# Kernel tuning notes

Hardware: AMD Instinct MI355X
Metric: run time of the kernel (lower is better)

The kernel has to match this reference:

```python
import jax, jax.numpy as jnp
import numpy as np

B, C, H, W = 16, 256, 32, 32
EPS = 1e-6


def setup_inputs() -> dict:
    key = jax.random.key(0)
    ks = jax.random.split(key, 6)
    s = 1.0 / np.sqrt(C)  # conv-like init scale
    return {
        "x": jax.random.normal(ks[0], (B, C, H, W), dtype=jnp.float32),
        "ln_w": jnp.ones((C,), dtype=jnp.float32),
        "ln_b": jnp.zeros((C,), dtype=jnp.float32),
        "wq": jax.random.normal(ks[1], (C, C), dtype=jnp.float32) * s,
        "bq": jnp.zeros((C,), dtype=jnp.float32),
        "wk": jax.random.normal(ks[2], (C, C), dtype=jnp.float32) * s,
        "bk": jnp.zeros((C,), dtype=jnp.float32),
        "wv": jax.random.normal(ks[3], (C, C), dtype=jnp.float32) * s,
        "bv": jnp.zeros((C,), dtype=jnp.float32),
        "wp": jax.random.normal(ks[4], (C, C), dtype=jnp.float32) * s,
        "bp": jnp.zeros((C,), dtype=jnp.float32),
    }


def reference(x, ln_w, ln_b, wq, bq, wk, bk, wv, bv, wp, bp):
    b, c, h, w = x.shape
    n = h * w
    # LayerNorm2d: normalize over channel dim (biased variance)
    mean = jnp.mean(x, axis=1, keepdims=True)
    var = jnp.var(x, axis=1, keepdims=True)
    hn = (x - mean) / jnp.sqrt(var + EPS)
    hn = hn * ln_w[None, :, None, None] + ln_b[None, :, None, None]
    hn = hn.reshape(b, c, n)  # [B, C, N]
    # 1x1 convs == channel matmuls; tokens layout [B, N, C]
    q = jnp.einsum('oc,bcn->bno', wq, hn) + bq  # [B, N, C]
    k = jnp.einsum('oc,bcn->bon', wk, hn) + bk[None, :, None]  # [B, C, N]
    v = jnp.einsum('oc,bcn->bno', wv, hn) + bv  # [B, N, C]
    scale = c ** (-0.5)
    attn = jnp.einsum('bnc,bcm->bnm', q, k) * scale  # [B, N, N]
    attn = jax.nn.softmax(attn, axis=-1)
    # dropout is identity in eval mode (deterministic reference)
    out = jnp.einsum('bnm,bmc->bnc', attn, v)  # [B, N, C]
    out = jnp.einsum('oc,bnc->bon', wp, out) + bp[None, :, None]  # [B, C, N]
    out = out.reshape(b, c, h, w)
    return x + out
```

## Files before the change

kernel.cpp:

```cpp
#include <hip/hip_runtime.h>
#include <hip/hip_bf16.h>
#include <stdint.h>
#include <math.h>

typedef __attribute__((ext_vector_type(8))) short bf8_t;
typedef __attribute__((ext_vector_type(4))) float f4_t;
typedef __attribute__((ext_vector_type(16))) float f16x_t;
typedef __attribute__((ext_vector_type(2))) unsigned u32x2;
typedef unsigned short u16;

#define GLOAD16(g, l) __builtin_amdgcn_global_load_lds(                                  \
    (const __attribute__((address_space(1))) void*)(g),                                  \
    (__attribute__((address_space(3))) void*)(l), 16, 0, 0)

#define KEEPALIVE(v) asm volatile("" : "+v"(v))

#define QSCALE 0.090168444f

__device__ __forceinline__ u16 f2bf(float f) {
    union { float f; unsigned u; } c; c.f = f;
    unsigned u = c.u;
    return (u16)((u + 0x7fffu + ((u >> 16) & 1u)) >> 16);
}

__device__ __forceinline__ unsigned cvt_pk_bf16(float lo, float hi_) {
    unsigned r;
    asm("v_cvt_pk_bf16_f32 %0, %1, %2" : "=v"(r) : "v"(lo), "v"(hi_));
    return r;
}

__device__ __forceinline__ void plswap(unsigned& a, unsigned& b) {
    u32x2 r = __builtin_amdgcn_permlane32_swap(a, b, false, false);
    a = r[0]; b = r[1];
}

__device__ __forceinline__ void pack_frags(const unsigned* pw, bf8_t& f0v, bf8_t& f1v) {
    unsigned w0 = pw[0], w1 = pw[1], w2 = pw[2], w3 = pw[3];
    unsigned u0 = pw[4], u1 = pw[5], u2 = pw[6], u3 = pw[7];
    plswap(w2, w0);
    plswap(w3, w1);
    plswap(u2, u0);
    plswap(u3, u1);
    union { unsigned w[4]; bf8_t v; } f0, f1;
    f0.w[0] = w0; f0.w[1] = w1; f0.w[2] = w2; f0.w[3] = w3;
    f1.w[0] = u0; f1.w[1] = u1; f1.w[2] = u2; f1.w[3] = u3;
    f0v = f0.v; f1v = f1.v;
}

__global__ void prep_kernel(const float* __restrict__ wq, const float* __restrict__ wk,
                            const float* __restrict__ wv, const float* __restrict__ wp,
                            const float* __restrict__ bq, const float* __restrict__ bk,
                            const float* __restrict__ bv,
                            u16* __restrict__ wcatT, u16* __restrict__ wpt,
                            float* __restrict__ biasc) {
    int idx = blockIdx.x * 256 + threadIdx.x;
    if (idx < 196608) {
        int o = idx >> 8, c = idx & 255;
        float v = (o < 256) ? wq[o * 256 + c]
                : (o < 512) ? wk[(o - 256) * 256 + c]
                            : wv[(o - 512) * 256 + c];
        wcatT[(((c >> 3) * 768) + o) * 8 + (c & 7)] = f2bf(v);
    } else if (idx < 262144) {
        int i = idx - 196608;
        int o = i >> 8, d = i & 255;
        wpt[(((d >> 3) * 256) + o) * 8 + (d & 7)] = f2bf(wp[i]);
    } else if (idx < 262912) {
        int i = idx - 262144;
        biasc[i] = (i < 256) ? bq[i] : (i < 512) ? bk[i - 256] : bv[i - 512];
    }
}

__global__ __launch_bounds__(256) void lnqkv_kernel(
    const float* __restrict__ x, const float* __restrict__ lw,
    const float* __restrict__ lb,
    const u16* __restrict__ wcatT, const float* __restrict__ biasc,
    u16* __restrict__ qbuf, u16* __restrict__ ktp, u16* __restrict__ vtp) {
    __shared__ u16 hn_lds[32 * 32 * 8];
    __shared__ float2 red[8][32];

    const int tid = threadIdx.x;
    const int bid = blockIdx.x;
    const int b = bid >> 5, n0 = (bid & 31) * 32;
    const int tok = tid & 31, cpart = tid >> 5;

    const float* xb = x + (size_t)b * 262144 + n0 + tok;
    float v[32];
    float s = 0.f, s2 = 0.f;
    #pragma unroll
    for (int i = 0; i < 32; i++) {
        v[i] = xb[(size_t)(cpart * 32 + i) * 1024];
        s += v[i]; s2 += v[i] * v[i];
    }
    red[cpart][tok] = make_float2(s, s2);
    __syncthreads();
    s = 0.f; s2 = 0.f;
    #pragma unroll
    for (int gi = 0; gi < 8; gi++) { float2 p = red[gi][tok]; s += p.x; s2 += p.y; }
    float mean = s * 0.00390625f;
    float rstd = rsqrtf(s2 * 0.00390625f - mean * mean + 1e-6f);
    #pragma unroll
    for (int j = 0; j < 4; j++) {
        bf8_t pk;
        #pragma unroll
        for (int e = 0; e < 8; e++) {
            int c = cpart * 32 + j * 8 + e;
            pk[e] = (short)f2bf((v[j * 8 + e] - mean) * rstd * lw[c] + lb[c]);
        }
        *(bf8_t*)&hn_lds[((cpart * 4 + j) * 32 + tok) * 8] = pk;
    }
    __syncthreads();

    const int lane = tid & 63, wv_ = tid >> 6;
    const int hi = lane >> 5, lq = lane & 31;
    const int n = n0 + lq;

    bf8_t hnf[16];
    #pragma unroll
    for (int tc = 0; tc < 16; tc++)
        hnf[tc] = *(const bf8_t*)&hn_lds[((tc * 2 + hi) * 32 + lq) * 8];
    #pragma unroll
    for (int tc = 0; tc < 16; tc++) KEEPALIVE(hnf[tc]);

    #pragma unroll
    for (int grp = 0; grp < 3; grp++) {
        #pragma unroll
        for (int sub = 0; sub < 2; sub++) {
            const int cb = grp * 256 + (wv_ * 2 + sub) * 32;
            bf8_t wf[16];
            #pragma unroll
            for (int tc = 0; tc < 16; tc++)
                wf[tc] = *(const bf8_t*)(wcatT + (((size_t)(tc * 2 + hi) * 768) + cb + lq) * 8);
            f16x_t acc = (f16x_t)0.0f;
            if (grp < 2) {
                #pragma unroll
                for (int tc = 0; tc < 16; tc++)
                    acc = __builtin_amdgcn_mfma_f32_32x32x16_bf16(wf[tc], hnf[tc], acc, 0, 0, 0);
                #pragma unroll
                for (int r = 0; r < 16; r++) {
                    float bv = biasc[cb + (r & 3) + 8 * (r >> 2) + 4 * hi];
                    acc[r] += bv;
                    if (grp == 0) acc[r] *= QSCALE;
                }
            } else {
                #pragma unroll
                for (int tc = 0; tc < 16; tc++)
                    acc = __builtin_amdgcn_mfma_f32_32x32x16_bf16(hnf[tc], wf[tc], acc, 0, 0, 0);
                float bv = biasc[cb + lq];
                #pragma unroll
                for (int r = 0; r < 16; r++) acc[r] += bv;
            }

            unsigned pw[8];
            #pragma unroll
            for (int j = 0; j < 8; j++) pw[j] = cvt_pk_bf16(acc[2 * j], acc[2 * j + 1]);
            bf8_t f0v, f1v;
            pack_frags(pw, f0v, f1v);

            if (grp == 0) {
                u16* qb = &qbuf[((size_t)b * 1024 + n) * 256 + cb];
                *(bf8_t*)(qb + hi * 8) = f0v;
                *(bf8_t*)(qb + 16 + hi * 8) = f1v;
            } else if (grp == 1) {
                int c0 = cb - 256 + hi * 8;
                *(bf8_t*)&ktp[(((size_t)b * 32 + (c0 >> 3)) * 1024 + n) * 8] = f0v;
                int c1 = c0 + 16;
                *(bf8_t*)&ktp[(((size_t)b * 32 + (c1 >> 3)) * 1024 + n) * 8] = f1v;
            } else {
                int d = cb - 512 + lq;
                int t0 = n0 + hi * 8;
                *(bf8_t*)&vtp[(((size_t)b * 128 + (t0 >> 3)) * 256 + d) * 8] = f0v;
                int t1 = t0 + 16;
                *(bf8_t*)&vtp[(((size_t)b * 128 + (t1 >> 3)) * 256 + d) * 8] = f1v;
            }
        }
    }
}

__global__ __launch_bounds__(512)
__attribute__((amdgpu_waves_per_eu(2, 2)))
void flash_kernel(const u16* __restrict__ qbuf,
                  const u16* __restrict__ kt,
                  const u16* __restrict__ vt3,
                  const u16* __restrict__ wpt,
                  const float* __restrict__ bp,
                  const float* __restrict__ x,
                  float* __restrict__ out) {
    __shared__ u16 K_lds[2][2][32 * 32 * 8];
    __shared__ u16 V_lds[2][2][4 * 256 * 8];
    __shared__ float lstat[2][32];

    const int flat = blockIdx.x;
    const int xcd = flat & 7, idx = flat >> 3;
    const int b = (xcd << 1) | (idx & 1);
    const int qb = idx >> 1;
    const int tid = threadIdx.x;
    const int wv = tid >> 6, lane = tid & 63;
    const int hi = lane >> 5, lq = lane & 31;
    const int qw = wv & 1, dw = (wv >> 1) & 1, g = wv >> 2;

    const int qrow = qb * 64 + qw * 32 + lq;
    const u16* qptr = qbuf + (size_t)(b * 1024 + qrow) * 256 + hi * 8;
    bf8_t qf[16];
    #pragma unroll
    for (int tc = 0; tc < 16; tc++) qf[tc] = *(const bf8_t*)(qptr + tc * 16);

    float l_r = 0.f;
    f16x_t o_acc[4];
    #pragma unroll
    for (int dt = 0; dt < 4; dt++) o_acc[dt] = (f16x_t)0.0f;

#define STAGE(T, BUF)                                                                     \
    {                                                                                     \
        _Pragma("unroll")                                                                 \
        for (int g2 = 0; g2 < 2; g2++) {                                                  \
            _Pragma("unroll")                                                             \
            for (int it = 0; it < 2; it++) {                                              \
                int cid = it * 512 + tid;                                                 \
                int chunk = cid >> 5, kvl = cid & 31;                                     \
                const u16* gk = kt + (((size_t)b * 32 + chunk) * 1024                     \
                                      + g2 * 512 + (T) * 32 + kvl) * 8;                   \
                GLOAD16(gk, &K_lds[g2][BUF][cid * 8]);                                    \
            }                                                                             \
            _Pragma("unroll")                                                             \
            for (int it = 0; it < 2; it++) {                                              \
                int cid = it * 512 + tid;                                                 \
                int kc = cid >> 8, d = cid & 255;                                         \
                const u16* gv = vt3 + (((size_t)b * 128 + g2 * 64 + (T) * 4 + kc) * 256   \
                                       + d) * 8;                                          \
                GLOAD16(gv, &V_lds[g2][BUF][cid * 8]);                                    \
            }                                                                             \
        }                                                                                 \
    }

    STAGE(0, 0);
    STAGE(1, 1);
    asm volatile("s_waitcnt vmcnt(8)" ::: "memory");
    __builtin_amdgcn_s_barrier();

    for (int t = 0; t < 16; ++t) {
        const int buf = t & 1;

        const u16* kb = &K_lds[g][buf][0];
        bf8_t kf[16];
        #pragma unroll
        for (int tc = 0; tc < 16; tc++)
            kf[tc] = *(const bf8_t*)(kb + ((tc * 2 + hi) * 32 + lq) * 8);
        #pragma unroll
        for (int tc = 0; tc < 16; tc++) KEEPALIVE(kf[tc]);

        f16x_t s0 = (f16x_t)0.0f, s1 = (f16x_t)0.0f;
        __builtin_amdgcn_s_setprio(1);
        #pragma unroll
        for (int tc = 0; tc < 8; tc++) {
            s0 = __builtin_amdgcn_mfma_f32_32x32x16_bf16(kf[2 * tc],     qf[2 * tc],     s0, 0, 0, 0);
            s1 = __builtin_amdgcn_mfma_f32_32x32x16_bf16(kf[2 * tc + 1], qf[2 * tc + 1], s1, 0, 0, 0);
        }
        __builtin_amdgcn_s_setprio(0);

        const u16* vb = &V_lds[g][buf][0];
        bf8_t vf[8];
        #pragma unroll
        for (int dt = 0; dt < 4; dt++) {
            int vrow = dw * 128 + dt * 32 + lq;
            vf[2 * dt]     = *(const bf8_t*)(vb + (hi * 256 + vrow) * 8);
            vf[2 * dt + 1] = *(const bf8_t*)(vb + ((2 + hi) * 256 + vrow) * 8);
        }
        #pragma unroll
        for (int j = 0; j < 8; j++) KEEPALIVE(vf[j]);

        f16x_t s = s0 + s1;

        float sum = 0.f;
        #pragma unroll
        for (int r = 0; r < 16; r++) { s[r] = exp2f(s[r]); sum += s[r]; }
        l_r += sum;

        unsigned pw[8];
        #pragma unroll
        for (int j = 0; j < 8; j++) pw[j] = cvt_pk_bf16(s[2 * j], s[2 * j + 1]);
        bf8_t f0v, f1v;
        pack_frags(pw, f0v, f1v);

        asm volatile("s_waitcnt lgkmcnt(0)" ::: "memory");
        __builtin_amdgcn_s_barrier();
        if (t < 14) STAGE(t + 2, buf);

        __builtin_amdgcn_s_setprio(1);
        #pragma unroll
        for (int dt = 0; dt < 4; dt++) {
            o_acc[dt] = __builtin_amdgcn_mfma_f32_32x32x16_bf16(vf[2 * dt],     f0v, o_acc[dt], 0, 0, 0);
            o_acc[dt] = __builtin_amdgcn_mfma_f32_32x32x16_bf16(vf[2 * dt + 1], f1v, o_acc[dt], 0, 0, 0);
        }
        __builtin_amdgcn_s_setprio(0);

        if (t < 15) {
            if (t < 14) { asm volatile("s_waitcnt vmcnt(8)" ::: "memory"); }
            else        { asm volatile("s_waitcnt vmcnt(0)" ::: "memory"); }
            __builtin_amdgcn_s_barrier();
        }
    }

    __syncthreads();

    float l_tot = l_r + __shfl_xor(l_r, 32);
    float* obuf = (float*)&K_lds[0][0][0];
    float* rb = obuf + (qw * 2 + dw) * 4096;
    if (g == 1) {
        #pragma unroll
        for (int dt = 0; dt < 4; dt++)
            #pragma unroll
            for (int r = 0; r < 16; r++) {
                int drow = dt * 32 + (r & 3) + 8 * (r >> 2) + 4 * hi;
                rb[drow * 32 + lq] = o_acc[dt][r];
            }
        if (dw == 0 && hi == 0) lstat[qw][lq] = l_tot;
    }
    __syncthreads();

    bf8_t wpf[16];
    #pragma unroll
    for (int tc = 0; tc < 16; tc++)
        wpf[tc] = *(const bf8_t*)(wpt + (((tc * 2 + hi) * 256) + wv * 32 + lq) * 8);

    u16* O16 = (u16*)&V_lds[0][0][0];
    if (g == 0) {
        float inv = 1.0f / (l_tot + lstat[qw][lq]);
        #pragma unroll
        for (int dt = 0; dt < 4; dt++)
            #pragma unroll
            for (int r = 0; r < 16; r++) {
                int drow = dt * 32 + (r & 3) + 8 * (r >> 2) + 4 * hi;
                int d = dw * 128 + drow;
                float val = (o_acc[dt][r] + rb[drow * 32 + lq]) * inv;
                O16[((d >> 3) * 64 + qw * 32 + lq) * 8 + (d & 7)] = f2bf(val);
            }
    }
    __syncthreads();

    f16x_t p0 = (f16x_t)0.0f, p1 = (f16x_t)0.0f;
    __builtin_amdgcn_s_setprio(1);
    #pragma unroll
    for (int tc = 0; tc < 16; tc++) {
        bf8_t of0 = *(const bf8_t*)(O16 + ((tc * 2 + hi) * 64 + lq) * 8);
        bf8_t of1 = *(const bf8_t*)(O16 + ((tc * 2 + hi) * 64 + 32 + lq) * 8);
        p0 = __builtin_amdgcn_mfma_f32_32x32x16_bf16(wpf[tc], of0, p0, 0, 0, 0);
        p1 = __builtin_amdgcn_mfma_f32_32x32x16_bf16(wpf[tc], of1, p1, 0, 0, 0);
    }
    __builtin_amdgcn_s_setprio(0);
    #pragma unroll
    for (int r = 0; r < 16; r++) {
        int crow = wv * 32 + (r & 3) + 8 * (r >> 2) + 4 * hi;
        size_t base = ((size_t)b * 256 + crow) * 1024 + qb * 64;
        float bpv = bp[crow];
        out[base + lq]      = p0[r] + bpv + x[base + lq];
        out[base + 32 + lq] = p1[r] + bpv + x[base + 32 + lq];
    }
#undef STAGE
}

extern "C" void kernel_launch(void* const* d_in, const int* in_sizes, int n_in,
                              void* d_out, int out_size, void* d_ws, size_t ws_size,
                              hipStream_t stream) {
    (void)in_sizes; (void)n_in; (void)out_size; (void)ws_size;
    const float* x   = (const float*)d_in[0];
    const float* lnw = (const float*)d_in[1];
    const float* lnb = (const float*)d_in[2];
    const float* wq  = (const float*)d_in[3];
    const float* bq  = (const float*)d_in[4];
    const float* wk  = (const float*)d_in[5];
    const float* bk  = (const float*)d_in[6];
    const float* wv  = (const float*)d_in[7];
    const float* bv  = (const float*)d_in[8];
    const float* wp  = (const float*)d_in[9];
    const float* bp  = (const float*)d_in[10];
    float* out = (float*)d_out;

    char* ws = (char*)d_ws;
    u16*   wcatT = (u16*)(ws);
    u16*   wpt   = (u16*)(ws + 0x60000);
    float* biasc = (float*)(ws + 0x80000);
    u16*   qbuf  = (u16*)(ws + 0x90000);
    u16*   kt    = (u16*)(ws + 0x890000);
    u16*   vt3   = (u16*)(ws + 0x1090000);

    prep_kernel<<<1028, 256, 0, stream>>>(wq, wk, wv, wp, bq, bk, bv, wcatT, wpt, biasc);
    lnqkv_kernel<<<512, 256, 0, stream>>>(x, lnw, lnb, wcatT, biasc, qbuf, kt, vt3);
    flash_kernel<<<256, 512, 0, stream>>>(qbuf, kt, vt3, wpt, bp, x, out);
}
```

Measured before the change: 67.14 us.

## Split flash kernel into 32-query blocks with 4 waves, drop KV split-reduction

Restructures the attention kernel from 256 blocks of 512 threads (64 queries, two KV halves combined through LDS) into 512 blocks of 256 threads, each handling 32 queries over the full KV range in 32 iterations. The cross-group partial-output reduction and its LDS round trip go away, and the grid has twice as many blocks to fill CUs, with two blocks allowed per CU. In exchange each block streams all K/V tiles itself, so K/V loads from L2 double. The output projection's weight fragments are also reloaded per block with half the reuse.

Measured after the change: 85.55 us. 27.4% more time.

```diff
diff --git a/kernel.cpp b/kernel.cpp
--- a/kernel.cpp
+++ b/kernel.cpp
@@ -176,8 +176,7 @@
     }
 }
 
-__global__ __launch_bounds__(512)
-__attribute__((amdgpu_waves_per_eu(2, 2)))
+__global__ __launch_bounds__(256, 2)
 void flash_kernel(const u16* __restrict__ qbuf,
                   const u16* __restrict__ kt,
                   const u16* __restrict__ vt3,
@@ -185,50 +184,42 @@
                   const float* __restrict__ bp,
                   const float* __restrict__ x,
                   float* __restrict__ out) {
-    __shared__ u16 K_lds[2][2][32 * 32 * 8];
-    __shared__ u16 V_lds[2][2][4 * 256 * 8];
-    __shared__ float lstat[2][32];
+    __shared__ u16 K_lds[2][32 * 32 * 8];
+    __shared__ u16 V_lds[2][4 * 256 * 8];
 
     const int flat = blockIdx.x;
     const int xcd = flat & 7, idx = flat >> 3;
     const int b = (xcd << 1) | (idx & 1);
-    const int qb = idx >> 1;
+    const int qt = idx >> 1;
     const int tid = threadIdx.x;
-    const int wv = tid >> 6, lane = tid & 63;
+    const int dw = tid >> 6, lane = tid & 63;
     const int hi = lane >> 5, lq = lane & 31;
-    const int qw = wv & 1, dw = (wv >> 1) & 1, g = wv >> 2;
-
-    const int qrow = qb * 64 + qw * 32 + lq;
+
+    const int qrow = qt * 32 + lq;
     const u16* qptr = qbuf + (size_t)(b * 1024 + qrow) * 256 + hi * 8;
     bf8_t qf[16];
     #pragma unroll
     for (int tc = 0; tc < 16; tc++) qf[tc] = *(const bf8_t*)(qptr + tc * 16);
 
     float l_r = 0.f;
-    f16x_t o_acc[4];
-    #pragma unroll
-    for (int dt = 0; dt < 4; dt++) o_acc[dt] = (f16x_t)0.0f;
+    f16x_t o_acc[2];
+    o_acc[0] = (f16x_t)0.0f; o_acc[1] = (f16x_t)0.0f;
 
 #define STAGE(T, BUF)                                                                     \
     {                                                                                     \
         _Pragma("unroll")                                                                 \
-        for (int g2 = 0; g2 < 2; g2++) {                                                  \
-            _Pragma("unroll")                                                             \
-            for (int it = 0; it < 2; it++) {                                              \
-                int cid = it * 512 + tid;                                                 \
-                int chunk = cid >> 5, kvl = cid & 31;                                     \
-                const u16* gk = kt + (((size_t)b * 32 + chunk) * 1024                     \
-                                      + g2 * 512 + (T) * 32 + kvl) * 8;                   \
-                GLOAD16(gk, &K_lds[g2][BUF][cid * 8]);                                    \
-            }                                                                             \
-            _Pragma("unroll")                                                             \
-            for (int it = 0; it < 2; it++) {                                              \
-                int cid = it * 512 + tid;                                                 \
-                int kc = cid >> 8, d = cid & 255;                                         \
-                const u16* gv = vt3 + (((size_t)b * 128 + g2 * 64 + (T) * 4 + kc) * 256   \
-                                       + d) * 8;                                          \
-                GLOAD16(gv, &V_lds[g2][BUF][cid * 8]);                                    \
-            }                                                                             \
+        for (int it = 0; it < 4; it++) {                                                  \
+            int cid = it * 256 + tid;                                                     \
+            int chunk = cid >> 5, kvl = cid & 31;                                         \
+            const u16* gk = kt + (((size_t)b * 32 + chunk) * 1024 + (T) * 32 + kvl) * 8;  \
+            GLOAD16(gk, &K_lds[BUF][cid * 8]);                                            \
+        }                                                                                 \
+        _Pragma("unroll")                                                                 \
+        for (int it = 0; it < 4; it++) {                                                  \
+            int cid = it * 256 + tid;                                                     \
+            int kc = cid >> 8, d = cid & 255;                                             \
+            const u16* gv = vt3 + (((size_t)b * 128 + (T) * 4 + kc) * 256 + d) * 8;       \
+            GLOAD16(gv, &V_lds[BUF][cid * 8]);                                            \
         }                                                                                 \
     }
 
@@ -237,10 +228,10 @@
     asm volatile("s_waitcnt vmcnt(8)" ::: "memory");
     __builtin_amdgcn_s_barrier();
 
-    for (int t = 0; t < 16; ++t) {
+    for (int t = 0; t < 32; ++t) {
         const int buf = t & 1;
 
-        const u16* kb = &K_lds[g][buf][0];
+        const u16* kb = &K_lds[buf][0];
         bf8_t kf[16];
         #pragma unroll
         for (int tc = 0; tc < 16; tc++)
@@ -257,16 +248,16 @@
         }
         __builtin_amdgcn_s_setprio(0);
 
-        const u16* vb = &V_lds[g][buf][0];
-        bf8_t vf[8];
-        #pragma unroll
-        for (int dt = 0; dt < 4; dt++) {
-            int vrow = dw * 128 + dt * 32 + lq;
+        const u16* vb = &V_lds[buf][0];
+        bf8_t vf[4];
+        #pragma unroll
+        for (int dt = 0; dt < 2; dt++) {
+            int vrow = dw * 64 + dt * 32 + lq;
             vf[2 * dt]     = *(const bf8_t*)(vb + (hi * 256 + vrow) * 8);
             vf[2 * dt + 1] = *(const bf8_t*)(vb + ((2 + hi) * 256 + vrow) * 8);
         }
         #pragma unroll
-        for (int j = 0; j < 8; j++) KEEPALIVE(vf[j]);
+        for (int j = 0; j < 4; j++) KEEPALIVE(vf[j]);
 
         f16x_t s = s0 + s1;
 
@@ -283,18 +274,18 @@
 
         asm volatile("s_waitcnt lgkmcnt(0)" ::: "memory");
         __builtin_amdgcn_s_barrier();
-        if (t < 14) STAGE(t + 2, buf);
+        if (t < 30) STAGE(t + 2, buf);
 
         __builtin_amdgcn_s_setprio(1);
         #pragma unroll
-        for (int dt = 0; dt < 4; dt++) {
+        for (int dt = 0; dt < 2; dt++) {
             o_acc[dt] = __builtin_amdgcn_mfma_f32_32x32x16_bf16(vf[2 * dt],     f0v, o_acc[dt], 0, 0, 0);
             o_acc[dt] = __builtin_amdgcn_mfma_f32_32x32x16_bf16(vf[2 * dt + 1], f1v, o_acc[dt], 0, 0, 0);
         }
         __builtin_amdgcn_s_setprio(0);
 
-        if (t < 15) {
-            if (t < 14) { asm volatile("s_waitcnt vmcnt(8)" ::: "memory"); }
+        if (t < 31) {
+            if (t < 30) { asm volatile("s_waitcnt vmcnt(8)" ::: "memory"); }
             else        { asm volatile("s_waitcnt vmcnt(0)" ::: "memory"); }
             __builtin_amdgcn_s_barrier();
         }
@@ -303,57 +294,39 @@
     __syncthreads();
 
     float l_tot = l_r + __shfl_xor(l_r, 32);
-    float* obuf = (float*)&K_lds[0][0][0];
-    float* rb = obuf + (qw * 2 + dw) * 4096;
-    if (g == 1) {
-        #pragma unroll
-        for (int dt = 0; dt < 4; dt++)
-            #pragma unroll
-            for (int r = 0; r < 16; r++) {
-                int drow = dt * 32 + (r & 3) + 8 * (r >> 2) + 4 * hi;
-                rb[drow * 32 + lq] = o_acc[dt][r];
-            }
-        if (dw == 0 && hi == 0) lstat[qw][lq] = l_tot;
-    }
+    float inv = 1.0f / l_tot;
+    u16* O16 = (u16*)&K_lds[0][0];
+    #pragma unroll
+    for (int dt = 0; dt < 2; dt++)
+        #pragma unroll
+        for (int r = 0; r < 16; r++) {
+            int drow = dt * 32 + (r & 3) + 8 * (r >> 2) + 4 * hi;
+            int d = dw * 64 + drow;
+            O16[((d >> 3) * 32 + lq) * 8 + (d & 7)] = f2bf(o_acc[dt][r] * inv);
+        }
     __syncthreads();
 
-    bf8_t wpf[16];
-    #pragma unroll
-    for (int tc = 0; tc < 16; tc++)
-        wpf[tc] = *(const bf8_t*)(wpt + (((tc * 2 + hi) * 256) + wv * 32 + lq) * 8);
-
-    u16* O16 = (u16*)&V_lds[0][0][0];
-    if (g == 0) {
-        float inv = 1.0f / (l_tot + lstat[qw][lq]);
-        #pragma unroll
-        for (int dt = 0; dt < 4; dt++)
-            #pragma unroll
-            for (int r = 0; r < 16; r++) {
-                int drow = dt * 32 + (r & 3) + 8 * (r >> 2) + 4 * hi;
-                int d = dw * 128 + drow;
-                float val = (o_acc[dt][r] + rb[drow * 32 + lq]) * inv;
-                O16[((d >> 3) * 64 + qw * 32 + lq) * 8 + (d & 7)] = f2bf(val);
-            }
-    }
-    __syncthreads();
-
-    f16x_t p0 = (f16x_t)0.0f, p1 = (f16x_t)0.0f;
-    __builtin_amdgcn_s_setprio(1);
-    #pragma unroll
-    for (int tc = 0; tc < 16; tc++) {
-        bf8_t of0 = *(const bf8_t*)(O16 + ((tc * 2 + hi) * 64 + lq) * 8);
-        bf8_t of1 = *(const bf8_t*)(O16 + ((tc * 2 + hi) * 64 + 32 + lq) * 8);
-        p0 = __builtin_amdgcn_mfma_f32_32x32x16_bf16(wpf[tc], of0, p0, 0, 0, 0);
-        p1 = __builtin_amdgcn_mfma_f32_32x32x16_bf16(wpf[tc], of1, p1, 0, 0, 0);
-    }
-    __builtin_amdgcn_s_setprio(0);
-    #pragma unroll
-    for (int r = 0; r < 16; r++) {
-        int crow = wv * 32 + (r & 3) + 8 * (r >> 2) + 4 * hi;
-        size_t base = ((size_t)b * 256 + crow) * 1024 + qb * 64;
-        float bpv = bp[crow];
-        out[base + lq]      = p0[r] + bpv + x[base + lq];
-        out[base + 32 + lq] = p1[r] + bpv + x[base + 32 + lq];
+    #pragma unroll
+    for (int cset = 0; cset < 2; cset++) {
+        const int cb = dw * 64 + cset * 32;
+        bf8_t wpf[16];
+        #pragma unroll
+        for (int tc = 0; tc < 16; tc++)
+            wpf[tc] = *(const bf8_t*)(wpt + (((tc * 2 + hi) * 256) + cb + lq) * 8);
+        f16x_t p = (f16x_t)0.0f;
+        __builtin_amdgcn_s_setprio(1);
+        #pragma unroll
+        for (int tc = 0; tc < 16; tc++) {
+            bf8_t of = *(const bf8_t*)(O16 + ((tc * 2 + hi) * 32 + lq) * 8);
+            p = __builtin_amdgcn_mfma_f32_32x32x16_bf16(wpf[tc], of, p, 0, 0, 0);
+        }
+        __builtin_amdgcn_s_setprio(0);
+        #pragma unroll
+        for (int r = 0; r < 16; r++) {
+            int crow = cb + (r & 3) + 8 * (r >> 2) + 4 * hi;
+            size_t base = ((size_t)b * 256 + crow) * 1024 + qt * 32;
+            out[base + lq] = p[r] + bp[crow] + x[base + lq];
+        }
     }
 #undef STAGE
 }
@@ -385,5 +358,5 @@
 
     prep_kernel<<<1028, 256, 0, stream>>>(wq, wk, wv, wp, bq, bk, bv, wcatT, wpt, biasc);
     lnqkv_kernel<<<512, 256, 0, stream>>>(x, lnw, lnb, wcatT, biasc, qbuf, kt, vt3);
-    flash_kernel<<<256, 512, 0, stream>>>(qbuf, kt, vt3, wpt, bp, x, out);
-}
+    flash_kernel<<<512, 256, 0, stream>>>(qbuf, kt, vt3, wpt, bp, x, out);
+}
```
